# Performance work log

Measured on AMD Instinct MI355X. Metric: run time of the kernel, lower is better.

## Reference

```python
import jax, jax.numpy as jnp
import numpy as np

HEADS = 8
DIM_HEAD = 40


def setup_inputs() -> dict:
    key = jax.random.key(0)
    ks = jax.random.split(key, 10)
    b, n, j, qd, cd = 8, 4096, 77, 320, 768
    inner = HEADS * DIM_HEAD  # 320
    x = jax.random.normal(ks[0], (b, n, qd), jnp.float32)
    embs = jax.random.normal(ks[1], (b, j, cd), jnp.float32)
    Wq = jax.random.normal(ks[2], (qd, inner), jnp.float32) * 0.02
    Wk = jax.random.normal(ks[3], (cd, inner), jnp.float32) * 0.02
    Wv = jax.random.normal(ks[4], (cd, inner), jnp.float32) * 0.02
    Wo = jax.random.normal(ks[5], (inner, qd), jnp.float32) * 0.02
    bo = jnp.zeros((qd,), jnp.float32)
    # per-query-token, per-key-token additive attention mask (float weights)
    cross_attn_mask = (jax.random.uniform(ks[6], (b, n, j)) < 0.5).astype(jnp.float32)
    strength = jnp.ones((1,), jnp.float32) * 0.8
    # captiontypes >= 0 marks valid key tokens; include some -1 (invalid)
    captiontypes = jax.random.randint(ks[7], (b, j), -1, 3).at[:, 0].set(0)
    global_prompt_mask = (jax.random.uniform(ks[8], (b, j)) > 0.05).at[:, 0].set(True)
    return {"x": x, "embs": embs, "Wq": Wq, "Wk": Wk, "Wv": Wv, "Wo": Wo,
            "bo": bo, "cross_attn_mask": cross_attn_mask, "strength": strength,
            "captiontypes": captiontypes, "global_prompt_mask": global_prompt_mask}


def _split_heads(t):
    # [b, n, h*d] -> [(b h), n, d], head index fastest (matches einops '(b h)')
    b, n, _ = t.shape
    return t.reshape(b, n, HEADS, DIM_HEAD).transpose(0, 2, 1, 3).reshape(b * HEADS, n, DIM_HEAD)


def reference(x, embs, Wq, Wk, Wv, Wo, bo, cross_attn_mask, strength,
              captiontypes, global_prompt_mask):
    b, n, _ = x.shape
    scale = DIM_HEAD ** -0.5
    q = _split_heads(x @ Wq).astype(jnp.float32)   # [(b h), n, d]
    k = _split_heads(embs @ Wk).astype(jnp.float32)  # [(b h), j, d]
    v = _split_heads(embs @ Wv)                      # [(b h), j, d]
    sim = jnp.einsum('bid,bjd->bij', q, k)           # [(b h), n, j] fp32

    NEG = -jnp.finfo(sim.dtype).max
    key_mask = captiontypes >= 0                     # [b, j]
    key_mask_bh = jnp.repeat(key_mask, HEADS, axis=0)[:, None, :]  # [(b h), 1, j]

    # masked std of sim over valid key positions (unbiased, ddof=1), no grad
    w = jnp.broadcast_to(key_mask_bh, sim.shape).astype(sim.dtype)
    cnt = jnp.sum(w)
    mean = jnp.sum(sim * w) / cnt
    var = jnp.sum(w * (sim - mean) ** 2) / (cnt - 1.0)
    simstd = jnp.sqrt(var)

    wf = cross_attn_mask * simstd * strength[0]      # [b, n, j]
    wf = jnp.where(global_prompt_mask[:, None, :], wf, NEG)
    wf = jnp.repeat(wf, HEADS, axis=0)               # [(b h), n, j]
    wf = jax.lax.stop_gradient(wf)

    sim = jnp.where(key_mask_bh, sim, NEG) + wf
    attn = jax.nn.softmax(sim * scale, axis=-1)
    out = jnp.einsum('bij,bjd->bid', attn, v)        # [(b h), n, d]
    out = out.reshape(b, HEADS, n, DIM_HEAD).transpose(0, 2, 1, 3).reshape(b, n, HEADS * DIM_HEAD)
    return out @ Wo + bo
```

## Files before the change

### kernel.cpp

```cpp
#include <hip/hip_runtime.h>
#include <hip/hip_bf16.h>
#include <math.h>

#define HEADS 8
#define DIMH 40
#define BB 8
#define NN 4096
#define JJ 77
#define CDIM 768
#define INNER 320
#define NEGF (-3.4028234663852886e38f)

using bf16 = __hip_bfloat16;
using f32x4 = __attribute__((ext_vector_type(4))) float;
using bf16x8 = __attribute__((ext_vector_type(8))) short;
using ushort8 = __attribute__((ext_vector_type(8))) unsigned short;
using ushort4v = __attribute__((ext_vector_type(4))) unsigned short;

__device__ __forceinline__ unsigned short f2u(float f){
    bf16 t = __float2bfloat16(f);
    return *reinterpret_cast<unsigned short*>(&t);
}
__device__ __forceinline__ float u2f(unsigned short u){
    unsigned int w = ((unsigned int)u) << 16;
    return __uint_as_float(w);
}

__global__ __launch_bounds__(256) void prep_weights(const float* __restrict__ Wq,
                                                    const float* __restrict__ Wo,
                                                    const float* __restrict__ Wk,
                                                    const float* __restrict__ Wv,
                                                    unsigned short* __restrict__ WqT,
                                                    unsigned short* __restrict__ WoT,
                                                    unsigned short* __restrict__ WkvT){
    __shared__ float tile[32][33];
    int blk = blockIdx.x;
    int tx = threadIdx.x & 31, ty = threadIdx.x >> 5;
    if(blk < 200){
        const float* in = (blk<100)? Wq : Wo;
        unsigned short* out = (blk<100)? WqT : WoT;
        int base = (blk<100)? blk : blk-100;
        int bx = base%10, by = base/10;
        int c0 = bx*32, r0 = by*32;
        #pragma unroll
        for(int i=0;i<32;i+=8) tile[ty+i][tx] = in[(size_t)(r0+ty+i)*320 + c0+tx];
        __syncthreads();
        #pragma unroll
        for(int i=0;i<32;i+=8) out[(size_t)(c0+ty+i)*320 + r0+tx] = f2u(tile[tx][ty+i]);
    } else {
        int local = blk-200;
        int nt = local%20, kt = local/20;
        int n0 = nt*32, k0 = kt*32;
        const float* in = (n0<320)? Wk : Wv;
        int nc0 = (n0<320)? n0 : n0-320;
        #pragma unroll
        for(int i=0;i<32;i+=8) tile[ty+i][tx] = in[(size_t)(k0+ty+i)*320 + nc0+tx];
        __syncthreads();
        #pragma unroll
        for(int i=0;i<32;i+=8) WkvT[(size_t)(n0+ty+i)*768 + k0+tx] = f2u(tile[tx][ty+i]);
    }
}

__global__ __launch_bounds__(256) void proj_kv_mfma(const float* __restrict__ embs,
                                                    const unsigned short* __restrict__ WkvT,
                                                    unsigned short* __restrict__ kws,
                                                    unsigned short* __restrict__ vt){
    __shared__ unsigned short As[64][40];
    __shared__ unsigned short Bs[64][40];
    int t = threadIdx.x;
    int bm = blockIdx.x % 10;
    int bn = blockIdx.x / 10;
    int row0 = bm*64, col0 = bn*64;
    int wave=t>>6, lane=t&63, l15=lane&15, lk=lane>>4;

    f32x4 acc[4];
    #pragma unroll
    for(int nf=0;nf<4;nf++) acc[nf]=(f32x4){0.f,0.f,0.f,0.f};

    for(int k0=0;k0<768;k0+=32){
        #pragma unroll
        for(int p=0;p<2;p++){
            int li = (p*256+t)*4; int r = li>>5, kk = li&31;
            int gr = row0 + r;
            ushort4v u;
            if(gr < 616){
                float4 v = *(const float4*)&embs[(size_t)gr*768 + k0+kk];
                u.x=f2u(v.x); u.y=f2u(v.y); u.z=f2u(v.z); u.w=f2u(v.w);
            } else { u.x=0;u.y=0;u.z=0;u.w=0; }
            *(ushort4v*)&As[r][kk] = u;
        }
        {
            int nn = t>>2, kk = (t&3)*8;
            *(ushort8*)&Bs[nn][kk] = *(const ushort8*)&WkvT[(size_t)(col0+nn)*768 + k0+kk];
        }
        __syncthreads();
        bf16x8 aF = *(const bf16x8*)&As[wave*16+l15][lk*8];
        #pragma unroll
        for(int nf=0;nf<4;nf++){
            bf16x8 bF = *(const bf16x8*)&Bs[nf*16+l15][lk*8];
            acc[nf] = __builtin_amdgcn_mfma_f32_16x16x32_bf16(aF,bF,acc[nf],0,0,0);
        }
        __syncthreads();
    }
    #pragma unroll
    for(int nf=0;nf<4;nf++){
        int col = col0 + nf*16 + l15;
        #pragma unroll
        for(int r=0;r<4;r++){
            int m = row0 + wave*16 + lk*4 + r;
            if(m < 616){
                int b = m/77, j = m - 77*b;
                unsigned short val = f2u(acc[nf][r]);
                if(col < 320){
                    int h = col/40, d = col - 40*h;
                    kws[(((size_t)b*HEADS+h)*JJ + j)*DIMH + d] = val;
                } else {
                    int c2 = col-320; int h = c2/40, d = c2 - 40*h;
                    size_t vbase = (((size_t)b*HEADS+h)*DIMH + d)*80;
                    vt[vbase + j] = val;
                    if(j==76){ vt[vbase+77]=0; vt[vbase+78]=0; vt[vbase+79]=0; }
                }
            }
        }
    }
}

__global__ __launch_bounds__(256) void gemm_q_stats(const float* __restrict__ x,
                                                    const unsigned short* __restrict__ WqT,
                                                    const unsigned short* __restrict__ kws,
                                                    const int* __restrict__ ct,
                                                    unsigned short* __restrict__ qh,
                                                    float2* __restrict__ partials){
    __shared__ unsigned short SH[256*80];
    unsigned short* As = SH;
    unsigned short* Bs = SH + 256*40;
    int t = threadIdx.x;
    int bm = blockIdx.x & 127;
    int bn = blockIdx.x >> 7;
    int row0 = bm*256, col0 = bn*80;
    int wave = t>>6, lane = t&63;
    int l15 = lane&15, lk = lane>>4;
    int b = row0 >> 12;
    bf16x8 zb = {0,0,0,0,0,0,0,0};

    f32x4 acc[4][5];
    #pragma unroll
    for(int i=0;i<4;i++)
        #pragma unroll
        for(int j=0;j<5;j++) acc[i][j] = (f32x4){0.f,0.f,0.f,0.f};

    for(int k0=0;k0<320;k0+=32){
        #pragma unroll
        for(int p=0;p<8;p++){
            int li = (p*256+t)*4; int r = li>>5, kk = li&31;
            float4 v = *(const float4*)&x[(size_t)(row0+r)*320 + k0+kk];
            ushort4v u; u.x=f2u(v.x); u.y=f2u(v.y); u.z=f2u(v.z); u.w=f2u(v.w);
            *(ushort4v*)&As[r*40+kk] = u;
        }
        #pragma unroll
        for(int p=0;p<2;p++){
            int idx = p*256+t;
            if(idx < 320){
                int nn = idx>>2, kk = (idx&3)*8;
                *(ushort8*)&Bs[nn*40+kk] = *(const ushort8*)&WqT[(size_t)(col0+nn)*320 + k0+kk];
            }
        }
        __syncthreads();
        bf16x8 a[4], bb[5];
        #pragma unroll
        for(int mf=0;mf<4;mf++) a[mf] = *(const bf16x8*)&As[(wave*64+mf*16+l15)*40 + lk*8];
        #pragma unroll
        for(int nf=0;nf<5;nf++) bb[nf] = *(const bf16x8*)&Bs[(nf*16+l15)*40 + lk*8];
        #pragma unroll
        for(int mf=0;mf<4;mf++)
            #pragma unroll
            for(int nf=0;nf<5;nf++)
                acc[mf][nf] = __builtin_amdgcn_mfma_f32_16x16x32_bf16(a[mf], bb[nf], acc[mf][nf], 0,0,0);
        __syncthreads();
    }
    #pragma unroll
    for(int mf=0;mf<4;mf++)
        #pragma unroll
        for(int nf=0;nf<5;nf++){
            int col = col0 + nf*16 + l15;
            int h = col/40, d = col - 40*h;
            int lcol = nf*16 + l15;
            #pragma unroll
            for(int r=0;r<4;r++){
                int lrow = wave*64 + mf*16 + lk*4 + r;
                int n = row0 + lrow - (b<<12);
                unsigned short v = f2u(acc[mf][nf][r]);
                qh[(((size_t)(b*8+h))*NN + n)*DIMH + d] = v;
                SH[lrow*80 + lcol] = v;
            }
        }
    __syncthreads();
    float s1=0.f, s2=0.f;
    #pragma unroll
    for(int h2=0;h2<2;h2++){
        int bh = b*8 + bn*2 + h2;
        bool kv[5]; bf16x8 bK0[5], bK1[5];
        #pragma unroll
        for(int jt=0;jt<5;jt++){
            int j = jt*16+l15;
            kv[jt] = (j<JJ) && (ct[b*JJ+j]>=0);
            bK0[jt] = (j<JJ) ? *(const bf16x8*)&kws[((size_t)bh*JJ+j)*DIMH + lk*8] : zb;
            bK1[jt] = (j<JJ && lk==0) ? *(const bf16x8*)&kws[((size_t)bh*JJ+j)*DIMH + 32] : zb;
        }
        #pragma unroll
        for(int mfq=0;mfq<4;mfq++){
            int wq = wave*64 + mfq*16;
            bf16x8 aF0 = *(const bf16x8*)&SH[(wq+l15)*80 + h2*40 + lk*8];
            bf16x8 aF1 = (lk==0) ? *(const bf16x8*)&SH[(wq+l15)*80 + h2*40 + 32] : zb;
            f32x4 sacc[5];
            #pragma unroll
            for(int jt=0;jt<5;jt++) sacc[jt]=(f32x4){0.f,0.f,0.f,0.f};
            #pragma unroll
            for(int jt=0;jt<5;jt++){
                sacc[jt] = __builtin_amdgcn_mfma_f32_16x16x32_bf16(aF0,bK0[jt],sacc[jt],0,0,0);
                sacc[jt] = __builtin_amdgcn_mfma_f32_16x16x32_bf16(aF1,bK1[jt],sacc[jt],0,0,0);
            }
            #pragma unroll
            for(int jt=0;jt<5;jt++){
                if(kv[jt]){
                    #pragma unroll
                    for(int r=0;r<4;r++){ float v=sacc[jt][r]; s1+=v; s2+=v*v; }
                }
            }
        }
    }
    #pragma unroll
    for(int off=32;off>0;off>>=1){ s1 += __shfl_down(s1,off); s2 += __shfl_down(s2,off); }
    __shared__ float sa[4], sb[4];
    if(lane==0){ sa[wave]=s1; sb[wave]=s2; }
    __syncthreads();
    if(t==0){
        partials[blockIdx.x] = make_float2(sa[0]+sa[1]+sa[2]+sa[3],
                                           sb[0]+sb[1]+sb[2]+sb[3]);
    }
}

template<int A_MODE, int C_MODE>
__global__ __launch_bounds__(256) void gemm_mfma(const void* __restrict__ A,
                                                 const unsigned short* __restrict__ Bt,
                                                 const float* __restrict__ bias,
                                                 void* __restrict__ C){
    __shared__ unsigned short As[256][40];
    __shared__ unsigned short Bs[64][40];
    int t = threadIdx.x;
    int bm = blockIdx.x & 127;
    int bn = blockIdx.x >> 7;
    int row0 = bm*256, col0 = bn*64;
    int wave = t>>6, lane = t&63;
    int l15 = lane&15, lk = lane>>4;

    f32x4 acc[4][4];
    #pragma unroll
    for(int i=0;i<4;i++)
        #pragma unroll
        for(int j=0;j<4;j++) acc[i][j] = (f32x4){0.f,0.f,0.f,0.f};

    for(int k0=0;k0<320;k0+=32){
        if(A_MODE==2){
            const unsigned short* Ab = (const unsigned short*)A;
            #pragma unroll
            for(int p=0;p<4;p++){
                int li = (p*256+t)*8; int r = li>>5, kk = li&31;
                int m = row0+r; int k = k0+kk;
                int b = m>>12, n = m&4095;
                int h = k/40, d = k-40*h;
                *(ushort8*)&As[r][kk] = *(const ushort8*)&Ab[(((size_t)(b*8+h))*NN + n)*DIMH + d];
            }
        } else {
            const float* Af = (const float*)A;
            #pragma unroll
            for(int p=0;p<8;p++){
                int li = (p*256+t)*4; int r = li>>5, kk = li&31;
                float4 v = *(const float4*)&Af[(size_t)(row0+r)*320 + k0+kk];
                ushort4v u; u.x=f2u(v.x); u.y=f2u(v.y); u.z=f2u(v.z); u.w=f2u(v.w);
                *(ushort4v*)&As[r][kk] = u;
            }
        }
        {
            int nn = t>>2, kk = (t&3)*8;
            *(ushort8*)&Bs[nn][kk] = *(const ushort8*)&Bt[(size_t)(col0+nn)*320 + k0+kk];
        }
        __syncthreads();
        bf16x8 a[4], b[4];
        #pragma unroll
        for(int mf=0;mf<4;mf++) a[mf] = *(const bf16x8*)&As[wave*64+mf*16+l15][lk*8];
        #pragma unroll
        for(int nf=0;nf<4;nf++) b[nf] = *(const bf16x8*)&Bs[nf*16+l15][lk*8];
        #pragma unroll
        for(int mf=0;mf<4;mf++)
            #pragma unroll
            for(int nf=0;nf<4;nf++)
                acc[mf][nf] = __builtin_amdgcn_mfma_f32_16x16x32_bf16(a[mf], b[nf], acc[mf][nf], 0,0,0);
        __syncthreads();
    }
    if(C_MODE==1){
        float* Cf = (float*)C;
        float bv[4];
        #pragma unroll
        for(int nf=0;nf<4;nf++) bv[nf] = bias[col0+nf*16+l15];
        #pragma unroll
        for(int mf=0;mf<4;mf++)
            #pragma unroll
            for(int nf=0;nf<4;nf++){
                int col = col0+nf*16+l15;
                #pragma unroll
                for(int r=0;r<4;r++){
                    int m = row0+wave*64+mf*16+lk*4+r;
                    Cf[(size_t)m*320+col] = acc[mf][nf][r] + bv[nf];
                }
            }
    } else {
        unsigned short* Cb = (unsigned short*)C;
        #pragma unroll
        for(int mf=0;mf<4;mf++)
            #pragma unroll
            for(int nf=0;nf<4;nf++){
                int col = col0+nf*16+l15;
                int h = col/40, d = col-40*h;
                #pragma unroll
                for(int r=0;r<4;r++){
                    int m = row0+wave*64+mf*16+lk*4+r;
                    int b = m>>12, n = m&4095;
                    Cb[(((size_t)(b*8+h))*NN + n)*DIMH + d] = f2u(acc[mf][nf][r]);
                }
            }
    }
}

__global__ __launch_bounds__(256) void attn_mfma(unsigned short* qh,
                                                 const unsigned short* __restrict__ kws,
                                                 const unsigned short* __restrict__ vt,
                                                 const float* __restrict__ cam,
                                                 const float* __restrict__ strength,
                                                 const int* __restrict__ ct,
                                                 const int* __restrict__ gpm,
                                                 const float2* __restrict__ partials){
    int bh = blockIdx.x;
    int b = bh>>3;
    __shared__ unsigned short P[64][104];
    __shared__ double da[4], db[4];
    __shared__ int scv[4], sgf[4];
    __shared__ float s_sim;
    __shared__ int s_gf;
    int t = threadIdx.x;
    int wave=t>>6, lane=t&63, l15=lane&15, lk=lane>>4;
    int wq0 = wave*16;
    bf16x8 zb = {0,0,0,0,0,0,0,0};
    ushort8 z8 = {0,0,0,0,0,0,0,0};

    int n0 = blockIdx.y*64;
    size_t qrow = ((size_t)bh*NN + n0 + wq0 + l15)*DIMH;
    bf16x8 aF0 = *(const bf16x8*)&qh[qrow + lk*8];
    bf16x8 aF1 = (lk==0) ? *(const bf16x8*)&qh[qrow + 32] : zb;
    float cv[5][4];
    #pragma unroll
    for(int jt=0;jt<5;jt++){
        int j = jt*16+l15; int jc = (j<JJ)? j : 76;
        #pragma unroll
        for(int r=0;r<4;r++){
            int row = n0 + wq0 + 4*lk + r;
            cv[jt][r] = cam[((size_t)b*NN+row)*JJ + jc];
        }
    }
    {
        double s1=0.0, s2=0.0;
        for(int i=t;i<512;i+=256){ float2 p = partials[i]; s1 += (double)p.x; s2 += (double)p.y; }
        int lcnt=0, lflag=0;
        for(int i=t;i<BB*JJ;i+=256){ if(ct[i]>=0) lcnt++; }
        for(int i=t;i<154;i+=256){ int g=gpm[i]; if(g!=0 && g!=1) lflag=1; }
        #pragma unroll
        for(int off=32;off>0;off>>=1){
            s1 += __shfl_down(s1,off); s2 += __shfl_down(s2,off);
            lcnt += __shfl_down(lcnt,off); lflag |= __shfl_down(lflag,off);
        }
        if(lane==0){ da[wave]=s1; db[wave]=s2; scv[wave]=lcnt; sgf[wave]=lflag; }
        __syncthreads();
        if(t==0){
            double S1 = da[0]+da[1]+da[2]+da[3];
            double S2 = db[0]+db[1]+db[2]+db[3];
            double cnt = (double)(scv[0]+scv[1]+scv[2]+scv[3]) * HEADS * NN;
            double var = (S2 - S1*S1/cnt)/(cnt-1.0);
            s_sim = (float)sqrt(var);
            s_gf = sgf[0]|sgf[1]|sgf[2]|sgf[3];
        }
    }
    if(t<64){ *(ushort8*)&P[t][80]=z8; *(ushort8*)&P[t][88]=z8; *(ushort8*)&P[t][96]=z8; }
    __syncthreads();
    float c = s_sim * strength[0];
    int gflag = s_gf;
    float km[5], gm[5], ad[5];
    #pragma unroll
    for(int jt=0;jt<5;jt++){
        int j = jt*16+l15;
        int kvv=0, gv=0;
        if(j<JJ){
            kvv = ct[b*JJ+j]>=0;
            gv = gflag ? (((const unsigned char*)gpm)[b*JJ+j]!=0) : (gpm[b*JJ+j]!=0);
        }
        km[jt] = (j<JJ && kvv)?1.f:0.f;
        ad[jt] = ((j<JJ && kvv)?0.f:NEGF) + ((j<JJ && gv)?0.f:NEGF);
        gm[jt] = (j<JJ && gv)? c : 0.f;
    }
    bf16x8 bK[2][5];
    #pragma unroll
    for(int ks=0;ks<2;ks++)
        #pragma unroll
        for(int jt=0;jt<5;jt++){
            int j = jt*16+l15;
            if(j<JJ && !(ks==1 && lk>=1))
                bK[ks][jt] = *(const bf16x8*)&kws[((size_t)bh*JJ + j)*DIMH + ks*32 + lk*8];
            else bK[ks][jt] = zb;
        }
    bf16x8 bV[3][3];
    #pragma unroll
    for(int ks=0;ks<3;ks++)
        #pragma unroll
        for(int nt=0;nt<3;nt++){
            int d = nt*16+l15;
            if(d<DIMH && !(ks==2 && lk>=2))
                bV[ks][nt] = *(const bf16x8*)&vt[((size_t)bh*DIMH + d)*80 + ks*32 + lk*8];
            else bV[ks][nt] = zb;
        }

    const float scale = 0.15811388300841897f;
    f32x4 sacc[5];
    #pragma unroll
    for(int jt=0;jt<5;jt++) sacc[jt]=(f32x4){0.f,0.f,0.f,0.f};
    #pragma unroll
    for(int jt=0;jt<5;jt++){
        sacc[jt] = __builtin_amdgcn_mfma_f32_16x16x32_bf16(aF0,bK[0][jt],sacc[jt],0,0,0);
        sacc[jt] = __builtin_amdgcn_mfma_f32_16x16x32_bf16(aF1,bK[1][jt],sacc[jt],0,0,0);
    }
    float lo[5][4];
    #pragma unroll
    for(int jt=0;jt<5;jt++){
        #pragma unroll
        for(int r=0;r<4;r++)
            lo[jt][r] = (sacc[jt][r]*km[jt] + cv[jt][r]*gm[jt] + ad[jt])*scale;
    }
    float dinv[4];
    #pragma unroll
    for(int r=0;r<4;r++){
        float m = lo[0][r];
        #pragma unroll
        for(int jt=1;jt<5;jt++) m = fmaxf(m, lo[jt][r]);
        #pragma unroll
        for(int msk=1;msk<16;msk<<=1) m = fmaxf(m, __shfl_xor(m,msk));
        float s=0.f;
        #pragma unroll
        for(int jt=0;jt<5;jt++){ float e=__expf(lo[jt][r]-m); lo[jt][r]=e; s+=e; }
        #pragma unroll
        for(int msk=1;msk<16;msk<<=1) s += __shfl_xor(s,msk);
        dinv[r]=1.f/s;
    }
    #pragma unroll
    for(int jt=0;jt<5;jt++){
        int j = jt*16+l15;
        #pragma unroll
        for(int r=0;r<4;r++) P[wq0+4*lk+r][j] = f2u(lo[jt][r]*dinv[r]);
    }
    __syncthreads();
    f32x4 oacc[3];
    #pragma unroll
    for(int nt=0;nt<3;nt++) oacc[nt]=(f32x4){0.f,0.f,0.f,0.f};
    #pragma unroll
    for(int ks=0;ks<3;ks++){
        bf16x8 aP = *(const bf16x8*)&P[wq0+l15][ks*32+lk*8];
        #pragma unroll
        for(int nt=0;nt<3;nt++)
            oacc[nt] = __builtin_amdgcn_mfma_f32_16x16x32_bf16(aP,bV[ks][nt],oacc[nt],0,0,0);
    }
    #pragma unroll
    for(int nt=0;nt<3;nt++){
        int d = nt*16+l15;
        #pragma unroll
        for(int r=0;r<4;r++){
            unsigned short ush = f2u(oacc[nt][r]);
            int other = __shfl_xor((int)ush, 1);
            if((l15&1)==0 && d<DIMH){
                unsigned int word = (unsigned int)ush | (((unsigned int)(unsigned short)other)<<16);
                int row = n0 + wq0 + 4*lk + r;
                *(unsigned int*)&qh[((size_t)bh*NN + row)*DIMH + d] = word;
            }
        }
    }
}

extern "C" void kernel_launch(void* const* d_in, const int* in_sizes, int n_in,
                              void* d_out, int out_size, void* d_ws, size_t ws_size,
                              hipStream_t stream) {
    const float* x        = (const float*)d_in[0];
    const float* embs     = (const float*)d_in[1];
    const float* Wq       = (const float*)d_in[2];
    const float* Wk       = (const float*)d_in[3];
    const float* Wv       = (const float*)d_in[4];
    const float* Wo       = (const float*)d_in[5];
    const float* bo       = (const float*)d_in[6];
    const float* cam      = (const float*)d_in[7];
    const float* strength = (const float*)d_in[8];
    const int*  ct       = (const int*)d_in[9];
    const int*  gpm      = (const int*)d_in[10];

    char* ws = (char*)d_ws;
    unsigned short* qh   = (unsigned short*)ws;
    unsigned short* kws  = (unsigned short*)(ws + 20971520);
    unsigned short* vt   = (unsigned short*)(ws + 21365760);
    unsigned short* WqT  = (unsigned short*)(ws + 21775360);
    unsigned short* WoT  = (unsigned short*)(ws + 21980160);
    unsigned short* WkvT = (unsigned short*)(ws + 22184960);
    float2* partials = (float2*)(ws + 23168000);

    prep_weights<<<680,256,0,stream>>>(Wq,Wo,Wk,Wv,WqT,WoT,WkvT);
    proj_kv_mfma<<<100,256,0,stream>>>(embs,WkvT,kws,vt);
    gemm_q_stats<<<512,256,0,stream>>>(x,WqT,kws,ct,qh,partials);
    attn_mfma<<<dim3(64,64),256,0,stream>>>(qh,kws,vt,cam,strength,ct,gpm,partials);
    gemm_mfma<2,1><<<640,256,0,stream>>>(qh,WoT,bo,d_out);
}
```

Measured before the change: 128.8 us.

## Hoist mask/std finalize into one kernel and share mask tile across two heads

```diff
diff --git a/kernel.cpp b/kernel.cpp
--- a/kernel.cpp
+++ b/kernel.cpp
@@ -240,6 +240,57 @@
     }
 }
 
+__global__ __launch_bounds__(256) void finalize_kernel(const float2* __restrict__ partials,
+                                                       const int* __restrict__ ct,
+                                                       const int* __restrict__ gpm,
+                                                       const float* __restrict__ strength,
+                                                       float* __restrict__ kmT,
+                                                       float* __restrict__ adT,
+                                                       float* __restrict__ gmT){
+    int t = threadIdx.x;
+    __shared__ int sflag, scnt;
+    if(t==0){ sflag=0; scnt=0; }
+    __syncthreads();
+    int lflag=0, lcnt=0;
+    for(int i=t;i<154;i+=256){ int g = gpm[i]; if(g!=0 && g!=1) lflag=1; }
+    for(int i=t;i<BB*JJ;i+=256){ if(ct[i]>=0) lcnt++; }
+    if(lflag) atomicOr(&sflag,1);
+    atomicAdd(&scnt,lcnt);
+    double s1=0.0, s2=0.0;
+    for(int i=t;i<512;i+=256){
+        float2 p = partials[i];
+        s1 += (double)p.x; s2 += (double)p.y;
+    }
+    #pragma unroll
+    for(int off=32;off>0;off>>=1){ s1 += __shfl_down(s1,off); s2 += __shfl_down(s2,off); }
+    __shared__ double da[4], db[4];
+    __shared__ float s_simstd;
+    int lane=t&63, w=t>>6;
+    if(lane==0){ da[w]=s1; db[w]=s2; }
+    __syncthreads();
+    if(t==0){
+        double S1 = da[0]+da[1]+da[2]+da[3];
+        double S2 = db[0]+db[1]+db[2]+db[3];
+        double cnt = (double)scnt * HEADS * NN;
+        double var = (S2 - S1*S1/cnt)/(cnt-1.0);
+        s_simstd = (float)sqrt(var);
+    }
+    __syncthreads();
+    float c = s_simstd * strength[0];
+    int gflag = sflag;
+    for(int i=t;i<BB*80;i+=256){
+        int b = i/80, j = i-80*b;
+        int kvv=0, gv=0;
+        if(j<JJ){
+            kvv = ct[b*JJ+j]>=0;
+            gv = gflag ? (((const unsigned char*)gpm)[b*JJ+j]!=0) : (gpm[b*JJ+j]!=0);
+        }
+        kmT[i] = (j<JJ && kvv)?1.f:0.f;
+        adT[i] = ((j<JJ && kvv)?0.f:NEGF) + ((j<JJ && gv)?0.f:NEGF);
+        gmT[i] = (j<JJ && gv)? c : 0.f;
+    }
+}
+
 template<int A_MODE, int C_MODE>
 __global__ __launch_bounds__(256) void gemm_mfma(const void* __restrict__ A,
                                                  const unsigned short* __restrict__ Bt,
@@ -314,21 +365,6 @@
                     Cf[(size_t)m*320+col] = acc[mf][nf][r] + bv[nf];
                 }
             }
-    } else {
-        unsigned short* Cb = (unsigned short*)C;
-        #pragma unroll
-        for(int mf=0;mf<4;mf++)
-            #pragma unroll
-            for(int nf=0;nf<4;nf++){
-                int col = col0+nf*16+l15;
-                int h = col/40, d = col-40*h;
-                #pragma unroll
-                for(int r=0;r<4;r++){
-                    int m = row0+wave*64+mf*16+lk*4+r;
-                    int b = m>>12, n = m&4095;
-                    Cb[(((size_t)(b*8+h))*NN + n)*DIMH + d] = f2u(acc[mf][nf][r]);
-                }
-            }
     }
 }
 
@@ -336,158 +372,129 @@
                                                  const unsigned short* __restrict__ kws,
                                                  const unsigned short* __restrict__ vt,
                                                  const float* __restrict__ cam,
-                                                 const float* __restrict__ strength,
-                                                 const int* __restrict__ ct,
-                                                 const int* __restrict__ gpm,
-                                                 const float2* __restrict__ partials){
-    int bh = blockIdx.x;
-    int b = bh>>3;
+                                                 const float* __restrict__ kmT,
+                                                 const float* __restrict__ adT,
+                                                 const float* __restrict__ gmT){
+    int bp = blockIdx.x;
+    int b = bp>>2, hp = bp&3;
+    int bh0 = b*8 + hp*2;
+    __shared__ unsigned short camS[64][80];
     __shared__ unsigned short P[64][104];
-    __shared__ double da[4], db[4];
-    __shared__ int scv[4], sgf[4];
-    __shared__ float s_sim;
-    __shared__ int s_gf;
     int t = threadIdx.x;
     int wave=t>>6, lane=t&63, l15=lane&15, lk=lane>>4;
     int wq0 = wave*16;
     bf16x8 zb = {0,0,0,0,0,0,0,0};
     ushort8 z8 = {0,0,0,0,0,0,0,0};
-
     int n0 = blockIdx.y*64;
-    size_t qrow = ((size_t)bh*NN + n0 + wq0 + l15)*DIMH;
-    bf16x8 aF0 = *(const bf16x8*)&qh[qrow + lk*8];
-    bf16x8 aF1 = (lk==0) ? *(const bf16x8*)&qh[qrow + 32] : zb;
-    float cv[5][4];
+
+    {
+        const float* csrc = cam + ((size_t)b*NN + n0)*JJ;
+        for(int idx=t; idx<64*JJ; idx+=256){
+            int r = idx/JJ, j = idx - r*JJ;
+            camS[r][j] = f2u(csrc[idx]);
+        }
+        for(int idx=t; idx<64*3; idx+=256){ int r=idx/3; camS[r][77+idx%3]=0; }
+    }
+    float km[5], gm[5], ad[5];
     #pragma unroll
     for(int jt=0;jt<5;jt++){
-        int j = jt*16+l15; int jc = (j<JJ)? j : 76;
-        #pragma unroll
-        for(int r=0;r<4;r++){
-            int row = n0 + wq0 + 4*lk + r;
-            cv[jt][r] = cam[((size_t)b*NN+row)*JJ + jc];
-        }
-    }
-    {
-        double s1=0.0, s2=0.0;
-        for(int i=t;i<512;i+=256){ float2 p = partials[i]; s1 += (double)p.x; s2 += (double)p.y; }
-        int lcnt=0, lflag=0;
-        for(int i=t;i<BB*JJ;i+=256){ if(ct[i]>=0) lcnt++; }
-        for(int i=t;i<154;i+=256){ int g=gpm[i]; if(g!=0 && g!=1) lflag=1; }
-        #pragma unroll
-        for(int off=32;off>0;off>>=1){
-            s1 += __shfl_down(s1,off); s2 += __shfl_down(s2,off);
-            lcnt += __shfl_down(lcnt,off); lflag |= __shfl_down(lflag,off);
-        }
-        if(lane==0){ da[wave]=s1; db[wave]=s2; scv[wave]=lcnt; sgf[wave]=lflag; }
-        __syncthreads();
-        if(t==0){
-            double S1 = da[0]+da[1]+da[2]+da[3];
-            double S2 = db[0]+db[1]+db[2]+db[3];
-            double cnt = (double)(scv[0]+scv[1]+scv[2]+scv[3]) * HEADS * NN;
-            double var = (S2 - S1*S1/cnt)/(cnt-1.0);
-            s_sim = (float)sqrt(var);
-            s_gf = sgf[0]|sgf[1]|sgf[2]|sgf[3];
-        }
+        int j = jt*16+l15;
+        km[jt] = kmT[b*80+j]; ad[jt] = adT[b*80+j]; gm[jt] = gmT[b*80+j];
     }
     if(t<64){ *(ushort8*)&P[t][80]=z8; *(ushort8*)&P[t][88]=z8; *(ushort8*)&P[t][96]=z8; }
     __syncthreads();
-    float c = s_sim * strength[0];
-    int gflag = s_gf;
-    float km[5], gm[5], ad[5];
-    #pragma unroll
-    for(int jt=0;jt<5;jt++){
-        int j = jt*16+l15;
-        int kvv=0, gv=0;
-        if(j<JJ){
-            kvv = ct[b*JJ+j]>=0;
-            gv = gflag ? (((const unsigned char*)gpm)[b*JJ+j]!=0) : (gpm[b*JJ+j]!=0);
-        }
-        km[jt] = (j<JJ && kvv)?1.f:0.f;
-        ad[jt] = ((j<JJ && kvv)?0.f:NEGF) + ((j<JJ && gv)?0.f:NEGF);
-        gm[jt] = (j<JJ && gv)? c : 0.f;
-    }
-    bf16x8 bK[2][5];
-    #pragma unroll
-    for(int ks=0;ks<2;ks++)
+
+    const float scale = 0.15811388300841897f;
+    for(int h2=0;h2<2;h2++){
+        int bh = bh0 + h2;
+        size_t qrow = ((size_t)bh*NN + n0 + wq0 + l15)*DIMH;
+        bf16x8 aF0 = *(const bf16x8*)&qh[qrow + lk*8];
+        bf16x8 aF1 = (lk==0) ? *(const bf16x8*)&qh[qrow + 32] : zb;
+        bf16x8 bK[2][5];
+        #pragma unroll
+        for(int ks=0;ks<2;ks++)
+            #pragma unroll
+            for(int jt=0;jt<5;jt++){
+                int j = jt*16+l15;
+                if(j<JJ && !(ks==1 && lk>=1))
+                    bK[ks][jt] = *(const bf16x8*)&kws[((size_t)bh*JJ + j)*DIMH + ks*32 + lk*8];
+                else bK[ks][jt] = zb;
+            }
+        bf16x8 bV[3][3];
+        #pragma unroll
+        for(int ks=0;ks<3;ks++)
+            #pragma unroll
+            for(int nt=0;nt<3;nt++){
+                int d = nt*16+l15;
+                if(d<DIMH && !(ks==2 && lk>=2))
+                    bV[ks][nt] = *(const bf16x8*)&vt[((size_t)bh*DIMH + d)*80 + ks*32 + lk*8];
+                else bV[ks][nt] = zb;
+            }
+        f32x4 sacc[5];
+        #pragma unroll
+        for(int jt=0;jt<5;jt++) sacc[jt]=(f32x4){0.f,0.f,0.f,0.f};
+        #pragma unroll
+        for(int jt=0;jt<5;jt++){
+            sacc[jt] = __builtin_amdgcn_mfma_f32_16x16x32_bf16(aF0,bK[0][jt],sacc[jt],0,0,0);
+            sacc[jt] = __builtin_amdgcn_mfma_f32_16x16x32_bf16(aF1,bK[1][jt],sacc[jt],0,0,0);
+        }
+        float lo[5][4];
         #pragma unroll
         for(int jt=0;jt<5;jt++){
             int j = jt*16+l15;
-            if(j<JJ && !(ks==1 && lk>=1))
-                bK[ks][jt] = *(const bf16x8*)&kws[((size_t)bh*JJ + j)*DIMH + ks*32 + lk*8];
-            else bK[ks][jt] = zb;
-        }
-    bf16x8 bV[3][3];
-    #pragma unroll
-    for(int ks=0;ks<3;ks++)
+            #pragma unroll
+            for(int r=0;r<4;r++){
+                float cvv = u2f(camS[wq0+4*lk+r][j]);
+                lo[jt][r] = (sacc[jt][r]*km[jt] + cvv*gm[jt] + ad[jt])*scale;
+            }
+        }
+        float dinv[4];
+        #pragma unroll
+        for(int r=0;r<4;r++){
+            float m = lo[0][r];
+            #pragma unroll
+            for(int jt=1;jt<5;jt++) m = fmaxf(m, lo[jt][r]);
+            #pragma unroll
+            for(int msk=1;msk<16;msk<<=1) m = fmaxf(m, __shfl_xor(m,msk));
+            float s=0.f;
+            #pragma unroll
+            for(int jt=0;jt<5;jt++){ float e=__expf(lo[jt][r]-m); lo[jt][r]=e; s+=e; }
+            #pragma unroll
+            for(int msk=1;msk<16;msk<<=1) s += __shfl_xor(s,msk);
+            dinv[r]=1.f/s;
+        }
+        #pragma unroll
+        for(int jt=0;jt<5;jt++){
+            int j = jt*16+l15;
+            #pragma unroll
+            for(int r=0;r<4;r++) P[wq0+4*lk+r][j] = f2u(lo[jt][r]*dinv[r]);
+        }
+        __syncthreads();
+        f32x4 oacc[3];
+        #pragma unroll
+        for(int nt=0;nt<3;nt++) oacc[nt]=(f32x4){0.f,0.f,0.f,0.f};
+        #pragma unroll
+        for(int ks=0;ks<3;ks++){
+            bf16x8 aP = *(const bf16x8*)&P[wq0+l15][ks*32+lk*8];
+            #pragma unroll
+            for(int nt=0;nt<3;nt++)
+                oacc[nt] = __builtin_amdgcn_mfma_f32_16x16x32_bf16(aP,bV[ks][nt],oacc[nt],0,0,0);
+        }
         #pragma unroll
         for(int nt=0;nt<3;nt++){
             int d = nt*16+l15;
-            if(d<DIMH && !(ks==2 && lk>=2))
-                bV[ks][nt] = *(const bf16x8*)&vt[((size_t)bh*DIMH + d)*80 + ks*32 + lk*8];
-            else bV[ks][nt] = zb;
-        }
-
-    const float scale = 0.15811388300841897f;
-    f32x4 sacc[5];
-    #pragma unroll
-    for(int jt=0;jt<5;jt++) sacc[jt]=(f32x4){0.f,0.f,0.f,0.f};
-    #pragma unroll
-    for(int jt=0;jt<5;jt++){
-        sacc[jt] = __builtin_amdgcn_mfma_f32_16x16x32_bf16(aF0,bK[0][jt],sacc[jt],0,0,0);
-        sacc[jt] = __builtin_amdgcn_mfma_f32_16x16x32_bf16(aF1,bK[1][jt],sacc[jt],0,0,0);
-    }
-    float lo[5][4];
-    #pragma unroll
-    for(int jt=0;jt<5;jt++){
-        #pragma unroll
-        for(int r=0;r<4;r++)
-            lo[jt][r] = (sacc[jt][r]*km[jt] + cv[jt][r]*gm[jt] + ad[jt])*scale;
-    }
-    float dinv[4];
-    #pragma unroll
-    for(int r=0;r<4;r++){
-        float m = lo[0][r];
-        #pragma unroll
-        for(int jt=1;jt<5;jt++) m = fmaxf(m, lo[jt][r]);
-        #pragma unroll
-        for(int msk=1;msk<16;msk<<=1) m = fmaxf(m, __shfl_xor(m,msk));
-        float s=0.f;
-        #pragma unroll
-        for(int jt=0;jt<5;jt++){ float e=__expf(lo[jt][r]-m); lo[jt][r]=e; s+=e; }
-        #pragma unroll
-        for(int msk=1;msk<16;msk<<=1) s += __shfl_xor(s,msk);
-        dinv[r]=1.f/s;
-    }
-    #pragma unroll
-    for(int jt=0;jt<5;jt++){
-        int j = jt*16+l15;
-        #pragma unroll
-        for(int r=0;r<4;r++) P[wq0+4*lk+r][j] = f2u(lo[jt][r]*dinv[r]);
-    }
-    __syncthreads();
-    f32x4 oacc[3];
-    #pragma unroll
-    for(int nt=0;nt<3;nt++) oacc[nt]=(f32x4){0.f,0.f,0.f,0.f};
-    #pragma unroll
-    for(int ks=0;ks<3;ks++){
-        bf16x8 aP = *(const bf16x8*)&P[wq0+l15][ks*32+lk*8];
-        #pragma unroll
-        for(int nt=0;nt<3;nt++)
-            oacc[nt] = __builtin_amdgcn_mfma_f32_16x16x32_bf16(aP,bV[ks][nt],oacc[nt],0,0,0);
-    }
-    #pragma unroll
-    for(int nt=0;nt<3;nt++){
-        int d = nt*16+l15;
-        #pragma unroll
-        for(int r=0;r<4;r++){
-            unsigned short ush = f2u(oacc[nt][r]);
-            int other = __shfl_xor((int)ush, 1);
-            if((l15&1)==0 && d<DIMH){
-                unsigned int word = (unsigned int)ush | (((unsigned int)(unsigned short)other)<<16);
-                int row = n0 + wq0 + 4*lk + r;
-                *(unsigned int*)&qh[((size_t)bh*NN + row)*DIMH + d] = word;
-            }
-        }
+            #pragma unroll
+            for(int r=0;r<4;r++){
+                unsigned short ush = f2u(oacc[nt][r]);
+                int other = __shfl_xor((int)ush, 1);
+                if((l15&1)==0 && d<DIMH){
+                    unsigned int word = (unsigned int)ush | (((unsigned int)(unsigned short)other)<<16);
+                    int row = n0 + wq0 + 4*lk + r;
+                    *(unsigned int*)&qh[((size_t)bh*NN + row)*DIMH + d] = word;
+                }
+            }
+        }
+        __syncthreads();
     }
 }
 
@@ -514,10 +521,14 @@
     unsigned short* WoT  = (unsigned short*)(ws + 21980160);
     unsigned short* WkvT = (unsigned short*)(ws + 22184960);
     float2* partials = (float2*)(ws + 23168000);
+    float* kmT = (float*)(ws + 23173120);
+    float* adT = (float*)(ws + 23175680);
+    float* gmT = (float*)(ws + 23178240);
 
     prep_weights<<<680,256,0,stream>>>(Wq,Wo,Wk,Wv,WqT,WoT,WkvT);
     proj_kv_mfma<<<100,256,0,stream>>>(embs,WkvT,kws,vt);
     gemm_q_stats<<<512,256,0,stream>>>(x,WqT,kws,ct,qh,partials);
-    attn_mfma<<<dim3(64,64),256,0,stream>>>(qh,kws,vt,cam,strength,ct,gpm,partials);
+    finalize_kernel<<<1,256,0,stream>>>(partials,ct,gpm,strength,kmT,adT,gmT);
+    attn_mfma<<<dim3(32,64),256,0,stream>>>(qh,kws,vt,cam,kmT,adT,gmT);
     gemm_mfma<2,1><<<640,256,0,stream>>>(qh,WoT,bo,d_out);
 }
```

Measured after the change: 123.3 us. 4.3% less time.
